# Kernel optimization log

Measured on AMD Instinct MI355X. Metric: run time of the kernel, lower is better.

The kernel has to match this reference:

```python
import jax, jax.numpy as jnp
import numpy as np

N = 20000      # nodes
E = 320000     # edges (before self loops)
DIN = 64       # input feature dim
C = 256        # hidden_dim (per-head channels)
HEADS = 4
NEG_SLOPE_ATT = 0.2   # GATv2 leaky_relu slope
NEG_SLOPE = 0.01      # torch F.leaky_relu default


def setup_inputs() -> dict:
    key = jax.random.key(0)
    ks = jax.random.split(key, 32)
    def g(i, shape, fan_in):
        return jax.random.normal(ks[i], shape, jnp.float32) * (1.0 / np.sqrt(fan_in))
    inp = {}
    inp["x"] = jax.random.normal(ks[0], (N, DIN), jnp.float32)
    inp["src"] = jax.random.randint(ks[1], (E,), 0, N, jnp.int32)
    inp["dst"] = jax.random.randint(ks[2], (E,), 0, N, jnp.int32)
    # input layer
    inp["W_in"] = g(3, (DIN, C), DIN); inp["b_in"] = jnp.zeros((C,), jnp.float32)
    # conv1: in=256 -> heads=4, out=256, concat
    inp["Wl1"] = g(4, (C, HEADS * C), C); inp["bl1"] = jnp.zeros((HEADS * C,), jnp.float32)
    inp["Wr1"] = g(5, (C, HEADS * C), C); inp["br1"] = jnp.zeros((HEADS * C,), jnp.float32)
    inp["att1"] = g(6, (HEADS, C), C); inp["bias1"] = jnp.zeros((HEADS * C,), jnp.float32)
    # conv2: in=1024 -> heads=4, out=256, concat
    inp["Wl2"] = g(7, (HEADS * C, HEADS * C), HEADS * C); inp["bl2"] = jnp.zeros((HEADS * C,), jnp.float32)
    inp["Wr2"] = g(8, (HEADS * C, HEADS * C), HEADS * C); inp["br2"] = jnp.zeros((HEADS * C,), jnp.float32)
    inp["att2"] = g(9, (HEADS, C), C); inp["bias2"] = jnp.zeros((HEADS * C,), jnp.float32)
    # conv3: in=1024 -> heads=1, out=256, no concat
    inp["Wl3"] = g(10, (HEADS * C, C), HEADS * C); inp["bl3"] = jnp.zeros((C,), jnp.float32)
    inp["Wr3"] = g(11, (HEADS * C, C), HEADS * C); inp["br3"] = jnp.zeros((C,), jnp.float32)
    inp["att3"] = g(12, (1, C), C); inp["bias3"] = jnp.zeros((C,), jnp.float32)
    # output layer
    inp["W_out"] = g(13, (C, 1), C); inp["b_out"] = jnp.zeros((1,), jnp.float32)
    return inp


def _seg_softmax(scores, seg, n):
    # scores: [E, H] segment-wise softmax over dst node ids
    m = jax.ops.segment_max(scores, seg, num_segments=n)
    ex = jnp.exp(scores - m[seg])
    den = jax.ops.segment_sum(ex, seg, num_segments=n)
    return ex / den[seg]


def _gatv2(x, s, d, Wl, bl, Wr, br, att, bias, heads, concat):
    n = x.shape[0]
    c = att.shape[1]
    xl = (x @ Wl + bl).reshape(n, heads, c)  # messages (source side)
    xr = (x @ Wr + br).reshape(n, heads, c)  # target side
    e = jax.nn.leaky_relu(xl[s] + xr[d], NEG_SLOPE_ATT)          # [E, H, C]
    sc = jnp.einsum('ehc,hc->eh', e, att)                         # [E, H]
    alpha = _seg_softmax(sc, d, n)                                # [E, H]
    out = jax.ops.segment_sum(alpha[:, :, None] * xl[s], d, num_segments=n)  # [N, H, C]
    out = out.reshape(n, heads * c) if concat else out.mean(axis=1)
    return out + bias


def reference(x, src, dst, W_in, b_in, Wl1, bl1, Wr1, br1, att1, bias1,
              Wl2, bl2, Wr2, br2, att2, bias2, Wl3, bl3, Wr3, br3, att3, bias3,
              W_out, b_out):
    n = x.shape[0]
    loop = jnp.arange(n, dtype=src.dtype)
    s = jnp.concatenate([src, loop])  # add_self_loops=True (PyG default)
    d = jnp.concatenate([dst, loop])
    h = jax.nn.leaky_relu(x @ W_in + b_in, NEG_SLOPE)
    h1 = jax.nn.elu(_gatv2(h, s, d, Wl1, bl1, Wr1, br1, att1, bias1, HEADS, True))
    h2 = jax.nn.elu(_gatv2(h1, s, d, Wl2, bl2, Wr2, br2, att2, bias2, HEADS, True))
    h3 = _gatv2(h2, s, d, Wl3, bl3, Wr3, br3, att3, bias3, 1, False)
    out = jax.nn.leaky_relu(h3, NEG_SLOPE) + h
    logits = (out @ W_out + b_out).squeeze(-1)
    return logits
```

## Files before the change

kernel.cpp:

```cpp
#include <hip/hip_runtime.h>
#include <math.h>

#define NEG_ATT 0.2f
#define NEG 0.01f

typedef __attribute__((ext_vector_type(8))) short short8;
typedef __attribute__((ext_vector_type(4))) float f32x4;

static __device__ __forceinline__ float lrelu(float x, float s) { return x > 0.f ? x : s * x; }
static __device__ __forceinline__ unsigned short f2b(float f) {
  union { float f; unsigned int i; } v; v.f = f;
  unsigned int r = (v.i + 0x7fffu + ((v.i >> 16) & 1u)) >> 16;
  return (unsigned short)r;
}
static __device__ __forceinline__ void unpack8(uint4 r, float* x) {
  union { unsigned int u; float f; } t;
  t.u = r.x << 16;          x[0] = t.f;
  t.u = r.x & 0xffff0000u;  x[1] = t.f;
  t.u = r.y << 16;          x[2] = t.f;
  t.u = r.y & 0xffff0000u;  x[3] = t.f;
  t.u = r.z << 16;          x[4] = t.f;
  t.u = r.z & 0xffff0000u;  x[5] = t.f;
  t.u = r.w << 16;          x[6] = t.f;
  t.u = r.w & 0xffff0000u;  x[7] = t.f;
}

__global__ void zero_int_kernel(int* __restrict__ p, int n) {
  int i = blockIdx.x * blockDim.x + threadIdx.x;
  if (i < n) p[i] = 0;
}

__global__ void hist_kernel(const int* __restrict__ dst, int* __restrict__ cnt, int E, int N) {
  int i = blockIdx.x * blockDim.x + threadIdx.x;
  int tot = E + N;
  if (i >= tot) return;
  int d = (i < E) ? dst[i] : (i - E);
  atomicAdd(&cnt[d], 1);
}

__global__ void scan_kernel(const int* __restrict__ cnt, int* __restrict__ rowptr,
                            int* __restrict__ cursor, int n) {
  __shared__ int wsum[16];
  __shared__ int carry_s;
  int t = threadIdx.x;
  int lane = t & 63, wv = t >> 6;
  if (t == 0) carry_s = 0;
  __syncthreads();
  for (int base = 0; base < n; base += 1024) {
    int i = base + t;
    int orig = (i < n) ? cnt[i] : 0;
    int v = orig;
    #pragma unroll
    for (int off = 1; off < 64; off <<= 1) {
      int u = __shfl_up(v, off);
      if (lane >= off) v += u;
    }
    if (lane == 63) wsum[wv] = v;
    __syncthreads();
    if (t < 16) {
      int s = wsum[t];
      #pragma unroll
      for (int off = 1; off < 16; off <<= 1) {
        int u = __shfl_up(s, off);
        if (t >= off) s += u;
      }
      wsum[t] = s;
    }
    __syncthreads();
    int waveoff = (wv > 0) ? wsum[wv - 1] : 0;
    int carry = carry_s;
    int excl = carry + waveoff + v - orig;
    if (i < n) { rowptr[i] = excl; cursor[i] = excl; }
    __syncthreads();
    if (t == 0) carry_s = carry + wsum[15];
    __syncthreads();
  }
  if (t == 0) rowptr[n] = carry_s;
}

__global__ void fill_kernel(const int* __restrict__ src, const int* __restrict__ dst,
                            int* __restrict__ cursor, int* __restrict__ colsrc, int E, int N) {
  int i = blockIdx.x * blockDim.x + threadIdx.x;
  int tot = E + N;
  if (i >= tot) return;
  int d, s;
  if (i < E) { d = dst[i]; s = src[i]; } else { d = i - E; s = i - E; }
  int pos = atomicAdd(&cursor[d], 1);
  colsrc[pos] = s;
}

__global__ __launch_bounds__(256) void transpose_w_bf16(
    const float* __restrict__ W, unsigned short* __restrict__ Wt, int K, int Ncol) {
  __shared__ float t[32][33];
  int n0 = blockIdx.x * 32, k0 = blockIdx.y * 32;
  int tx = threadIdx.x & 31, ty = threadIdx.x >> 5;
  #pragma unroll
  for (int i = 0; i < 4; ++i)
    t[ty + i * 8][tx] = W[(size_t)(k0 + ty + i * 8) * Ncol + n0 + tx];
  __syncthreads();
  #pragma unroll
  for (int i = 0; i < 4; ++i)
    Wt[(size_t)(n0 + ty + i * 8) * K + k0 + tx] = f2b(t[tx][ty + i * 8]);
}

__global__ void f2b_kernel(const float* __restrict__ in, unsigned short* __restrict__ out, int n) {
  int i = blockIdx.x * blockDim.x + threadIdx.x;
  if (i < n) out[i] = f2b(in[i]);
}

__global__ __launch_bounds__(256) void gemm_mfma(
    const unsigned short* __restrict__ A, const unsigned short* __restrict__ Bt,
    const float* __restrict__ bias, float* __restrict__ Cf, unsigned short* __restrict__ Cb,
    int M, int K, int ldcf, int ldcb, int act) {
  __shared__ __align__(16) unsigned short As[128 * 32];
  __shared__ __align__(16) unsigned short Bs[128 * 32];
  int tid = threadIdx.x;
  int wave = tid >> 6, lane = tid & 63;
  int wm = wave >> 1, wn = wave & 1;
  int quad = lane >> 4, l16 = lane & 15;
  int row0 = blockIdx.y * 128, col0 = blockIdx.x * 128;
  int r0 = tid >> 2, seg0 = tid & 3;
  int swz0 = r0 * 32 + ((seg0 ^ ((r0 >> 1) & 3)) * 8);
  int swz1 = swz0 + 64 * 32;
  int chunk = (quad ^ ((l16 >> 1) & 3)) * 8;

  const unsigned short* gA = A + (size_t)(row0 + r0) * K + seg0 * 8;
  const unsigned short* gB = Bt + (size_t)(col0 + r0) * K + seg0 * 8;
  const size_t rstep = (size_t)64 * K;

  f32x4 acc[4][4];
  #pragma unroll
  for (int i = 0; i < 4; ++i)
    #pragma unroll
    for (int j = 0; j < 4; ++j)
      acc[i][j] = (f32x4){0.f, 0.f, 0.f, 0.f};

  uint4 sa0 = *(const uint4*)(gA);
  uint4 sa1 = *(const uint4*)(gA + rstep);
  uint4 sb0 = *(const uint4*)(gB);
  uint4 sb1 = *(const uint4*)(gB + rstep);

  for (int k0 = 0; k0 < K; k0 += 32) {
    *(uint4*)&As[swz0] = sa0;
    *(uint4*)&As[swz1] = sa1;
    *(uint4*)&Bs[swz0] = sb0;
    *(uint4*)&Bs[swz1] = sb1;
    __syncthreads();
    int kn = k0 + 32;
    if (kn < K) {
      sa0 = *(const uint4*)(gA + kn);
      sa1 = *(const uint4*)(gA + kn + rstep);
      sb0 = *(const uint4*)(gB + kn);
      sb1 = *(const uint4*)(gB + kn + rstep);
    }
    short8 afr[4], bfr[4];
    #pragma unroll
    for (int t = 0; t < 4; ++t) {
      afr[t] = *(const short8*)&As[(wm * 64 + t * 16 + l16) * 32 + chunk];
      bfr[t] = *(const short8*)&Bs[(wn * 64 + t * 16 + l16) * 32 + chunk];
    }
    #pragma unroll
    for (int mt = 0; mt < 4; ++mt)
      #pragma unroll
      for (int nt = 0; nt < 4; ++nt)
        acc[mt][nt] = __builtin_amdgcn_mfma_f32_16x16x32_bf16(afr[mt], bfr[nt], acc[mt][nt], 0, 0, 0);
    __syncthreads();
  }

  #pragma unroll
  for (int mt = 0; mt < 4; ++mt) {
    #pragma unroll
    for (int r = 0; r < 4; ++r) {
      int row = row0 + wm * 64 + mt * 16 + quad * 4 + r;
      if (row >= M) continue;
      #pragma unroll
      for (int nt = 0; nt < 4; ++nt) {
        int col = col0 + wn * 64 + nt * 16 + l16;
        float v = acc[mt][nt][r] + bias[col];
        if (act == 1) v = lrelu(v, NEG);
        if (Cf) Cf[(size_t)row * ldcf + col] = v;
        if (Cb) Cb[(size_t)row * ldcb + col] = f2b(v);
      }
    }
  }
}

__global__ __launch_bounds__(256) void gat_agg_h4(
    const unsigned short* __restrict__ xlr,
    const int* __restrict__ rowptr, const int* __restrict__ colsrc,
    const float* __restrict__ att, const float* __restrict__ bias,
    unsigned short* __restrict__ outb, int n) {
  const int S = 2048, XROFF = 1024;
  int d = blockIdx.x;
  if (d >= n) return;
  int hd = threadIdx.x >> 6, ln = threadIdx.x & 63;
  int half = ln >> 5, l32 = ln & 31;
  int c0 = l32 * 8;
  float a[8], a5[8], xr_[8];
  {
    float4 t0 = *(const float4*)(att + hd * 256 + c0);
    float4 t1 = *(const float4*)(att + hd * 256 + c0 + 4);
    a[0]=t0.x; a[1]=t0.y; a[2]=t0.z; a[3]=t0.w;
    a[4]=t1.x; a[5]=t1.y; a[6]=t1.z; a[7]=t1.w;
    #pragma unroll
    for (int c = 0; c < 8; ++c) a5[c] = NEG_ATT * a[c];
    uint4 r = *(const uint4*)(xlr + (size_t)d * S + XROFF + hd * 256 + c0);
    unpack8(r, xr_);
  }
  float m = -1e30f, l = 0.f, acc[8];
  #pragma unroll
  for (int c = 0; c < 8; ++c) acc[c] = 0.f;
  int beg = rowptr[d], end = rowptr[d + 1];
  for (int j = beg; j < end; j += 2) {
    int jj = j + half;
    bool valid = (jj < end);
    int s = colsrc[valid ? jj : j];
    uint4 raw = *(const uint4*)(xlr + (size_t)s * S + hd * 256 + c0);
    float x[8];
    unpack8(raw, x);
    float p = 0.f;
    #pragma unroll
    for (int c = 0; c < 8; ++c) {
      float u = x[c] + xr_[c];
      p = fmaf(u, (u > 0.f ? a[c] : a5[c]), p);
    }
    #pragma unroll
    for (int off = 16; off >= 1; off >>= 1) p += __shfl_xor(p, off);
    if (!valid) p = -1e30f;
    float nm = fmaxf(m, p);
    if (nm > m) {
      float scl = __expf(m - nm);
      l *= scl;
      #pragma unroll
      for (int c = 0; c < 8; ++c) acc[c] *= scl;
      m = nm;
    }
    float w = __expf(p - m);
    l += w;
    #pragma unroll
    for (int c = 0; c < 8; ++c) acc[c] = fmaf(w, x[c], acc[c]);
  }
  float mo = __shfl_xor(m, 32);
  float lo = __shfl_xor(l, 32);
  float M = fmaxf(m, mo);
  float sl = __expf(m - M);
  float so = __expf(mo - M);
  float L = fmaf(l, sl, lo * so);
  float inv = 1.f / L;
  float4 b0 = *(const float4*)(bias + hd * 256 + c0);
  float4 b1 = *(const float4*)(bias + hd * 256 + c0 + 4);
  float bb[8] = {b0.x, b0.y, b0.z, b0.w, b1.x, b1.y, b1.z, b1.w};
  unsigned int ou[4];
  #pragma unroll
  for (int c = 0; c < 8; ++c) {
    float po = __shfl_xor(acc[c], 32);
    float v = fmaf(acc[c], sl, po * so) * inv + bb[c];
    v = v > 0.f ? v : expm1f(v);
    unsigned int bv = (unsigned int)f2b(v);
    if (c & 1) ou[c >> 1] |= bv << 16; else ou[c >> 1] = bv;
  }
  if (half == 0) {
    uint4 o = make_uint4(ou[0], ou[1], ou[2], ou[3]);
    *(uint4*)(outb + (size_t)d * 1024 + hd * 256 + c0) = o;
  }
}

__global__ __launch_bounds__(256) void gat_agg_h1(
    const unsigned short* __restrict__ xlr,
    const int* __restrict__ rowptr, const int* __restrict__ colsrc,
    const float* __restrict__ att, const float* __restrict__ bias,
    float* __restrict__ out, int n) {
  const int S = 512, XROFF = 256;
  int wv = threadIdx.x >> 6, ln = threadIdx.x & 63;
  int d = blockIdx.x * 4 + wv;
  if (d >= n) return;
  int half = ln >> 5, l32 = ln & 31;
  int c0 = l32 * 8;
  float a[8], a5[8], xr_[8];
  {
    float4 t0 = *(const float4*)(att + c0);
    float4 t1 = *(const float4*)(att + c0 + 4);
    a[0]=t0.x; a[1]=t0.y; a[2]=t0.z; a[3]=t0.w;
    a[4]=t1.x; a[5]=t1.y; a[6]=t1.z; a[7]=t1.w;
    #pragma unroll
    for (int c = 0; c < 8; ++c) a5[c] = NEG_ATT * a[c];
    uint4 r = *(const uint4*)(xlr + (size_t)d * S + XROFF + c0);
    unpack8(r, xr_);
  }
  float m = -1e30f, l = 0.f, acc[8];
  #pragma unroll
  for (int c = 0; c < 8; ++c) acc[c] = 0.f;
  int beg = rowptr[d], end = rowptr[d + 1];
  for (int j = beg; j < end; j += 2) {
    int jj = j + half;
    bool valid = (jj < end);
    int s = colsrc[valid ? jj : j];
    uint4 raw = *(const uint4*)(xlr + (size_t)s * S + c0);
    float x[8];
    unpack8(raw, x);
    float p = 0.f;
    #pragma unroll
    for (int c = 0; c < 8; ++c) {
      float u = x[c] + xr_[c];
      p = fmaf(u, (u > 0.f ? a[c] : a5[c]), p);
    }
    #pragma unroll
    for (int off = 16; off >= 1; off >>= 1) p += __shfl_xor(p, off);
    if (!valid) p = -1e30f;
    float nm = fmaxf(m, p);
    if (nm > m) {
      float scl = __expf(m - nm);
      l *= scl;
      #pragma unroll
      for (int c = 0; c < 8; ++c) acc[c] *= scl;
      m = nm;
    }
    float w = __expf(p - m);
    l += w;
    #pragma unroll
    for (int c = 0; c < 8; ++c) acc[c] = fmaf(w, x[c], acc[c]);
  }
  float mo = __shfl_xor(m, 32);
  float lo = __shfl_xor(l, 32);
  float M = fmaxf(m, mo);
  float sl = __expf(m - M);
  float so = __expf(mo - M);
  float L = fmaf(l, sl, lo * so);
  float inv = 1.f / L;
  float4 b0 = *(const float4*)(bias + c0);
  float4 b1 = *(const float4*)(bias + c0 + 4);
  float bb[8] = {b0.x, b0.y, b0.z, b0.w, b1.x, b1.y, b1.z, b1.w};
  float ov[8];
  #pragma unroll
  for (int c = 0; c < 8; ++c) {
    float po = __shfl_xor(acc[c], 32);
    ov[c] = fmaf(acc[c], sl, po * so) * inv + bb[c];
  }
  if (half == 0) {
    float4 o0 = {ov[0], ov[1], ov[2], ov[3]};
    float4 o1 = {ov[4], ov[5], ov[6], ov[7]};
    *(float4*)(out + (size_t)d * 256 + c0) = o0;
    *(float4*)(out + (size_t)d * 256 + c0 + 4) = o1;
  }
}

__global__ __launch_bounds__(256) void final_logits(
    const float* __restrict__ h3, const float* __restrict__ h,
    const float* __restrict__ Wout, const float* __restrict__ bout,
    float* __restrict__ out, int n) {
  int wv = threadIdx.x >> 6, ln = threadIdx.x & 63;
  int node = blockIdx.x * 4 + wv;
  if (node >= n) return;
  int c0 = ln * 4;
  float4 a = *(const float4*)(h3 + (size_t)node * 256 + c0);
  float4 b = *(const float4*)(h + (size_t)node * 256 + c0);
  float4 w = *(const float4*)(Wout + c0);
  float vx = lrelu(a.x, NEG) + b.x;
  float vy = lrelu(a.y, NEG) + b.y;
  float vz = lrelu(a.z, NEG) + b.z;
  float vw = lrelu(a.w, NEG) + b.w;
  float v = vx * w.x + vy * w.y + vz * w.z + vw * w.w;
  #pragma unroll
  for (int off = 32; off >= 1; off >>= 1) v += __shfl_xor(v, off);
  if (ln == 0) out[node] = v + bout[0];
}

extern "C" void kernel_launch(void* const* d_in, const int* in_sizes, int n_in,
                              void* d_out, int out_size, void* d_ws, size_t ws_size,
                              hipStream_t stream) {
  const float* x    = (const float*)d_in[0];
  const int*   src  = (const int*)d_in[1];
  const int*   dst  = (const int*)d_in[2];
  const float* W_in = (const float*)d_in[3];
  const float* b_in = (const float*)d_in[4];
  const float* Wl1 = (const float*)d_in[5];  const float* bl1 = (const float*)d_in[6];
  const float* Wr1 = (const float*)d_in[7];  const float* br1 = (const float*)d_in[8];
  const float* att1 = (const float*)d_in[9]; const float* bias1 = (const float*)d_in[10];
  const float* Wl2 = (const float*)d_in[11]; const float* bl2 = (const float*)d_in[12];
  const float* Wr2 = (const float*)d_in[13]; const float* br2 = (const float*)d_in[14];
  const float* att2 = (const float*)d_in[15]; const float* bias2 = (const float*)d_in[16];
  const float* Wl3 = (const float*)d_in[17]; const float* bl3 = (const float*)d_in[18];
  const float* Wr3 = (const float*)d_in[19]; const float* br3 = (const float*)d_in[20];
  const float* att3 = (const float*)d_in[21]; const float* bias3 = (const float*)d_in[22];
  const float* W_out = (const float*)d_in[23]; const float* b_out = (const float*)d_in[24];

  const int N = in_sizes[0] / 64;
  const int E = in_sizes[1];
  const int NP = ((N + 127) / 128) * 128;
  float* out = (float*)d_out;

  char* p = (char*)d_ws;
  float* h   = (float*)p;            p += (size_t)N * 256 * 4;
  float* h3  = (float*)p;            p += (size_t)N * 256 * 4;
  unsigned short* xbf  = (unsigned short*)p; p += (size_t)NP * 64 * 2;
  unsigned short* hbf  = (unsigned short*)p; p += (size_t)NP * 256 * 2;
  unsigned short* h1bf = (unsigned short*)p; p += (size_t)NP * 1024 * 2;
  unsigned short* h2bf = (unsigned short*)p; p += (size_t)NP * 1024 * 2;
  unsigned short* xlr  = (unsigned short*)p; p += (size_t)N * 2048 * 2;
  unsigned short* WtIn  = (unsigned short*)p; p += (size_t)256 * 64 * 2;
  unsigned short* WtLR1 = (unsigned short*)p; p += (size_t)2048 * 256 * 2;
  unsigned short* WtLR2 = (unsigned short*)p; p += (size_t)2048 * 1024 * 2;
  unsigned short* WtLR3 = (unsigned short*)p; p += (size_t)512 * 1024 * 2;
  float* bLR1 = (float*)p;           p += (size_t)2048 * 4;
  float* bLR2 = (float*)p;           p += (size_t)2048 * 4;
  float* bLR3 = (float*)p;           p += (size_t)512 * 4;
  int* cnt    = (int*)p;             p += (size_t)N * 4;
  int* cursor = (int*)p;             p += (size_t)N * 4;
  int* rowptr = (int*)p;             p += (size_t)(N + 1) * 4;
  int* colsrc = (int*)p;

  const int tot = E + N;
  dim3 blk(256);

  zero_int_kernel<<<(N + 255) / 256, blk, 0, stream>>>(cnt, N);
  hist_kernel<<<(tot + 255) / 256, blk, 0, stream>>>(dst, cnt, E, N);
  scan_kernel<<<1, 1024, 0, stream>>>(cnt, rowptr, cursor, N);
  fill_kernel<<<(tot + 255) / 256, blk, 0, stream>>>(src, dst, cursor, colsrc, E, N);

  transpose_w_bf16<<<dim3(8, 2), blk, 0, stream>>>(W_in, WtIn, 64, 256);
  transpose_w_bf16<<<dim3(32, 8), blk, 0, stream>>>(Wl1, WtLR1, 256, 1024);
  transpose_w_bf16<<<dim3(32, 8), blk, 0, stream>>>(Wr1, WtLR1 + (size_t)1024 * 256, 256, 1024);
  transpose_w_bf16<<<dim3(32, 32), blk, 0, stream>>>(Wl2, WtLR2, 1024, 1024);
  transpose_w_bf16<<<dim3(32, 32), blk, 0, stream>>>(Wr2, WtLR2 + (size_t)1024 * 1024, 1024, 1024);
  transpose_w_bf16<<<dim3(8, 32), blk, 0, stream>>>(Wl3, WtLR3, 1024, 256);
  transpose_w_bf16<<<dim3(8, 32), blk, 0, stream>>>(Wr3, WtLR3 + (size_t)256 * 1024, 1024, 256);
  f2b_kernel<<<(N * 64 + 255) / 256, blk, 0, stream>>>(x, xbf, N * 64);

  hipMemcpyAsync(bLR1, bl1, 1024 * 4, hipMemcpyDeviceToDevice, stream);
  hipMemcpyAsync(bLR1 + 1024, br1, 1024 * 4, hipMemcpyDeviceToDevice, stream);
  hipMemcpyAsync(bLR2, bl2, 1024 * 4, hipMemcpyDeviceToDevice, stream);
  hipMemcpyAsync(bLR2 + 1024, br2, 1024 * 4, hipMemcpyDeviceToDevice, stream);
  hipMemcpyAsync(bLR3, bl3, 256 * 4, hipMemcpyDeviceToDevice, stream);
  hipMemcpyAsync(bLR3 + 256, br3, 256 * 4, hipMemcpyDeviceToDevice, stream);

  int gy = NP / 128;
  int gagg4 = N;
  int gagg1 = (N + 3) / 4;

  gemm_mfma<<<dim3(2, gy), blk, 0, stream>>>(xbf, WtIn, b_in, h, hbf, N, 64, 256, 256, 1);

  gemm_mfma<<<dim3(16, gy), blk, 0, stream>>>(hbf, WtLR1, bLR1, nullptr, xlr, N, 256, 0, 2048, 0);
  gat_agg_h4<<<gagg4, blk, 0, stream>>>(xlr, rowptr, colsrc, att1, bias1, h1bf, N);

  gemm_mfma<<<dim3(16, gy), blk, 0, stream>>>(h1bf, WtLR2, bLR2, nullptr, xlr, N, 1024, 0, 2048, 0);
  gat_agg_h4<<<gagg4, blk, 0, stream>>>(xlr, rowptr, colsrc, att2, bias2, h2bf, N);

  gemm_mfma<<<dim3(4, gy), blk, 0, stream>>>(h2bf, WtLR3, bLR3, nullptr, xlr, N, 1024, 0, 512, 0);
  gat_agg_h1<<<gagg1, blk, 0, stream>>>(xlr, rowptr, colsrc, att3, bias3, h3, N);

  final_logits<<<gagg1, blk, 0, stream>>>(h3, h, W_out, b_out, out, N);
}
```

Measured before the change: 784.2 us.

## Fuse prep kernels, widen GEMM K-tile to 64, fuse final logits into aggregation

Weight transposes, bias copies and x conversion are merged into one launch, replacing eight kernels and six memcpys. The MFMA GEMM now stages a 64-wide K slice per iteration, halving barrier and loop overhead at the cost of doubled LDS and more prefetch registers. The last GAT aggregation directly computes the residual, leaky-relu and output dot product, removing the h3 intermediate buffer and a separate kernel.

```diff
diff --git a/kernel.cpp b/kernel.cpp
--- a/kernel.cpp
+++ b/kernel.cpp
@@ -89,10 +89,12 @@
   colsrc[pos] = s;
 }
 
-__global__ __launch_bounds__(256) void transpose_w_bf16(
-    const float* __restrict__ W, unsigned short* __restrict__ Wt, int K, int Ncol) {
-  __shared__ float t[32][33];
-  int n0 = blockIdx.x * 32, k0 = blockIdx.y * 32;
+static __device__ __forceinline__ void do_transpose(
+    const float* __restrict__ W, unsigned short* __restrict__ Wt,
+    int K, int Ncol, int lbid, float (*t)[33]) {
+  int nxb = Ncol >> 5;
+  int bx = lbid % nxb, by = lbid / nxb;
+  int n0 = bx * 32, k0 = by * 32;
   int tx = threadIdx.x & 31, ty = threadIdx.x >> 5;
   #pragma unroll
   for (int i = 0; i < 4; ++i)
@@ -103,26 +105,61 @@
     Wt[(size_t)(n0 + ty + i * 8) * K + k0 + tx] = f2b(t[tx][ty + i * 8]);
 }
 
-__global__ void f2b_kernel(const float* __restrict__ in, unsigned short* __restrict__ out, int n) {
-  int i = blockIdx.x * blockDim.x + threadIdx.x;
-  if (i < n) out[i] = f2b(in[i]);
+__global__ __launch_bounds__(256) void prep_all(
+    const float* __restrict__ W_in,
+    const float* __restrict__ Wl1, const float* __restrict__ Wr1,
+    const float* __restrict__ Wl2, const float* __restrict__ Wr2,
+    const float* __restrict__ Wl3, const float* __restrict__ Wr3,
+    unsigned short* __restrict__ WtIn,
+    unsigned short* __restrict__ WtL1, unsigned short* __restrict__ WtR1,
+    unsigned short* __restrict__ WtL2, unsigned short* __restrict__ WtR2,
+    unsigned short* __restrict__ WtL3, unsigned short* __restrict__ WtR3,
+    const float* __restrict__ x, unsigned short* __restrict__ xbf, int nx_elems,
+    const float* __restrict__ bl1, const float* __restrict__ br1,
+    const float* __restrict__ bl2, const float* __restrict__ br2,
+    const float* __restrict__ bl3, const float* __restrict__ br3,
+    float* __restrict__ bLR1, float* __restrict__ bLR2, float* __restrict__ bLR3) {
+  __shared__ float t[32][33];
+  int bid = blockIdx.x;
+  if (bid < 16)        { do_transpose(W_in, WtIn, 64, 256, bid, t); return; }
+  if (bid < 272)       { do_transpose(Wl1, WtL1, 256, 1024, bid - 16, t); return; }
+  if (bid < 528)       { do_transpose(Wr1, WtR1, 256, 1024, bid - 272, t); return; }
+  if (bid < 1552)      { do_transpose(Wl2, WtL2, 1024, 1024, bid - 528, t); return; }
+  if (bid < 2576)      { do_transpose(Wr2, WtR2, 1024, 1024, bid - 1552, t); return; }
+  if (bid < 2832)      { do_transpose(Wl3, WtL3, 1024, 256, bid - 2576, t); return; }
+  if (bid < 3088)      { do_transpose(Wr3, WtR3, 1024, 256, bid - 2832, t); return; }
+  if (bid < 3106) {
+    int i = (bid - 3088) * 256 + threadIdx.x;
+    if (i < 1024)      bLR1[i] = bl1[i];
+    else if (i < 2048) bLR1[i] = br1[i - 1024];
+    else if (i < 3072) bLR2[i - 2048] = bl2[i - 2048];
+    else if (i < 4096) bLR2[i - 2048] = br2[i - 3072];
+    else if (i < 4352) bLR3[i - 4096] = bl3[i - 4096];
+    else if (i < 4608) bLR3[i - 4096] = br3[i - 4352];
+    return;
+  }
+  int i = (bid - 3106) * 256 + threadIdx.x;
+  if (i < nx_elems) xbf[i] = f2b(x[i]);
 }
 
 __global__ __launch_bounds__(256) void gemm_mfma(
     const unsigned short* __restrict__ A, const unsigned short* __restrict__ Bt,
     const float* __restrict__ bias, float* __restrict__ Cf, unsigned short* __restrict__ Cb,
     int M, int K, int ldcf, int ldcb, int act) {
-  __shared__ __align__(16) unsigned short As[128 * 32];
-  __shared__ __align__(16) unsigned short Bs[128 * 32];
+  __shared__ __align__(16) unsigned short As[128 * 64];
+  __shared__ __align__(16) unsigned short Bs[128 * 64];
   int tid = threadIdx.x;
   int wave = tid >> 6, lane = tid & 63;
   int wm = wave >> 1, wn = wave & 1;
   int quad = lane >> 4, l16 = lane & 15;
   int row0 = blockIdx.y * 128, col0 = blockIdx.x * 128;
   int r0 = tid >> 2, seg0 = tid & 3;
-  int swz0 = r0 * 32 + ((seg0 ^ ((r0 >> 1) & 3)) * 8);
-  int swz1 = swz0 + 64 * 32;
-  int chunk = (quad ^ ((l16 >> 1) & 3)) * 8;
+  int swz = (seg0 ^ ((r0 >> 1) & 3)) * 8;
+  int wsl0 = r0 * 64 + swz;
+  int wsl1 = wsl0 + 32;
+  int wsl2 = wsl0 + 64 * 64;
+  int wsl3 = wsl2 + 32;
+  int chunkbase = (quad ^ ((l16 >> 1) & 3)) * 8;
 
   const unsigned short* gA = A + (size_t)(row0 + r0) * K + seg0 * 8;
   const unsigned short* gB = Bt + (size_t)(col0 + r0) * K + seg0 * 8;
@@ -135,35 +172,50 @@
     for (int j = 0; j < 4; ++j)
       acc[i][j] = (f32x4){0.f, 0.f, 0.f, 0.f};
 
-  uint4 sa0 = *(const uint4*)(gA);
-  uint4 sa1 = *(const uint4*)(gA + rstep);
-  uint4 sb0 = *(const uint4*)(gB);
-  uint4 sb1 = *(const uint4*)(gB + rstep);
-
-  for (int k0 = 0; k0 < K; k0 += 32) {
-    *(uint4*)&As[swz0] = sa0;
-    *(uint4*)&As[swz1] = sa1;
-    *(uint4*)&Bs[swz0] = sb0;
-    *(uint4*)&Bs[swz1] = sb1;
-    __syncthreads();
-    int kn = k0 + 32;
+  uint4 pa0 = *(const uint4*)(gA);
+  uint4 pa1 = *(const uint4*)(gA + 32);
+  uint4 pa2 = *(const uint4*)(gA + rstep);
+  uint4 pa3 = *(const uint4*)(gA + rstep + 32);
+  uint4 pb0 = *(const uint4*)(gB);
+  uint4 pb1 = *(const uint4*)(gB + 32);
+  uint4 pb2 = *(const uint4*)(gB + rstep);
+  uint4 pb3 = *(const uint4*)(gB + rstep + 32);
+
+  for (int k0 = 0; k0 < K; k0 += 64) {
+    *(uint4*)&As[wsl0] = pa0;
+    *(uint4*)&As[wsl1] = pa1;
+    *(uint4*)&As[wsl2] = pa2;
+    *(uint4*)&As[wsl3] = pa3;
+    *(uint4*)&Bs[wsl0] = pb0;
+    *(uint4*)&Bs[wsl1] = pb1;
+    *(uint4*)&Bs[wsl2] = pb2;
+    *(uint4*)&Bs[wsl3] = pb3;
+    __syncthreads();
+    int kn = k0 + 64;
     if (kn < K) {
-      sa0 = *(const uint4*)(gA + kn);
-      sa1 = *(const uint4*)(gA + kn + rstep);
-      sb0 = *(const uint4*)(gB + kn);
-      sb1 = *(const uint4*)(gB + kn + rstep);
-    }
-    short8 afr[4], bfr[4];
-    #pragma unroll
-    for (int t = 0; t < 4; ++t) {
-      afr[t] = *(const short8*)&As[(wm * 64 + t * 16 + l16) * 32 + chunk];
-      bfr[t] = *(const short8*)&Bs[(wn * 64 + t * 16 + l16) * 32 + chunk];
-    }
-    #pragma unroll
-    for (int mt = 0; mt < 4; ++mt)
-      #pragma unroll
-      for (int nt = 0; nt < 4; ++nt)
-        acc[mt][nt] = __builtin_amdgcn_mfma_f32_16x16x32_bf16(afr[mt], bfr[nt], acc[mt][nt], 0, 0, 0);
+      pa0 = *(const uint4*)(gA + kn);
+      pa1 = *(const uint4*)(gA + kn + 32);
+      pa2 = *(const uint4*)(gA + kn + rstep);
+      pa3 = *(const uint4*)(gA + kn + rstep + 32);
+      pb0 = *(const uint4*)(gB + kn);
+      pb1 = *(const uint4*)(gB + kn + 32);
+      pb2 = *(const uint4*)(gB + kn + rstep);
+      pb3 = *(const uint4*)(gB + kn + rstep + 32);
+    }
+    #pragma unroll
+    for (int h = 0; h < 2; ++h) {
+      short8 afr[4], bfr[4];
+      #pragma unroll
+      for (int t = 0; t < 4; ++t) {
+        afr[t] = *(const short8*)&As[(wm * 64 + t * 16 + l16) * 64 + h * 32 + chunkbase];
+        bfr[t] = *(const short8*)&Bs[(wn * 64 + t * 16 + l16) * 64 + h * 32 + chunkbase];
+      }
+      #pragma unroll
+      for (int mt = 0; mt < 4; ++mt)
+        #pragma unroll
+        for (int nt = 0; nt < 4; ++nt)
+          acc[mt][nt] = __builtin_amdgcn_mfma_f32_16x16x32_bf16(afr[mt], bfr[nt], acc[mt][nt], 0, 0, 0);
+    }
     __syncthreads();
   }
 
@@ -265,11 +317,12 @@
   }
 }
 
-__global__ __launch_bounds__(256) void gat_agg_h1(
+__global__ __launch_bounds__(256) void gat_agg_h1_final(
     const unsigned short* __restrict__ xlr,
     const int* __restrict__ rowptr, const int* __restrict__ colsrc,
     const float* __restrict__ att, const float* __restrict__ bias,
-    float* __restrict__ out, int n) {
+    const float* __restrict__ h, const float* __restrict__ Wout,
+    const float* __restrict__ bout, float* __restrict__ out, int n) {
   const int S = 512, XROFF = 256;
   int wv = threadIdx.x >> 6, ln = threadIdx.x & 63;
   int d = blockIdx.x * 4 + wv;
@@ -330,39 +383,21 @@
   float4 b0 = *(const float4*)(bias + c0);
   float4 b1 = *(const float4*)(bias + c0 + 4);
   float bb[8] = {b0.x, b0.y, b0.z, b0.w, b1.x, b1.y, b1.z, b1.w};
-  float ov[8];
+  float4 h0 = *(const float4*)(h + (size_t)d * 256 + c0);
+  float4 h1v = *(const float4*)(h + (size_t)d * 256 + c0 + 4);
+  float hh[8] = {h0.x, h0.y, h0.z, h0.w, h1v.x, h1v.y, h1v.z, h1v.w};
+  float4 w0 = *(const float4*)(Wout + c0);
+  float4 w1 = *(const float4*)(Wout + c0 + 4);
+  float ww[8] = {w0.x, w0.y, w0.z, w0.w, w1.x, w1.y, w1.z, w1.w};
+  float v = 0.f;
   #pragma unroll
   for (int c = 0; c < 8; ++c) {
-    float po = __shfl_xor(acc[c], 32);
-    ov[c] = fmaf(acc[c], sl, po * so) * inv + bb[c];
-  }
-  if (half == 0) {
-    float4 o0 = {ov[0], ov[1], ov[2], ov[3]};
-    float4 o1 = {ov[4], ov[5], ov[6], ov[7]};
-    *(float4*)(out + (size_t)d * 256 + c0) = o0;
-    *(float4*)(out + (size_t)d * 256 + c0 + 4) = o1;
-  }
-}
-
-__global__ __launch_bounds__(256) void final_logits(
-    const float* __restrict__ h3, const float* __restrict__ h,
-    const float* __restrict__ Wout, const float* __restrict__ bout,
-    float* __restrict__ out, int n) {
-  int wv = threadIdx.x >> 6, ln = threadIdx.x & 63;
-  int node = blockIdx.x * 4 + wv;
-  if (node >= n) return;
-  int c0 = ln * 4;
-  float4 a = *(const float4*)(h3 + (size_t)node * 256 + c0);
-  float4 b = *(const float4*)(h + (size_t)node * 256 + c0);
-  float4 w = *(const float4*)(Wout + c0);
-  float vx = lrelu(a.x, NEG) + b.x;
-  float vy = lrelu(a.y, NEG) + b.y;
-  float vz = lrelu(a.z, NEG) + b.z;
-  float vw = lrelu(a.w, NEG) + b.w;
-  float v = vx * w.x + vy * w.y + vz * w.z + vw * w.w;
-  #pragma unroll
-  for (int off = 32; off >= 1; off >>= 1) v += __shfl_xor(v, off);
-  if (ln == 0) out[node] = v + bout[0];
+    float h3c = fmaf(acc[c], sl, __shfl_xor(acc[c], 32) * so) * inv + bb[c];
+    v = fmaf(lrelu(h3c, NEG) + hh[c], ww[c], v);
+  }
+  #pragma unroll
+  for (int off = 16; off >= 1; off >>= 1) v += __shfl_xor(v, off);
+  if (ln == 0) out[d] = v + bout[0];
 }
 
 extern "C" void kernel_launch(void* const* d_in, const int* in_sizes, int n_in,
@@ -391,7 +426,6 @@
 
   char* p = (char*)d_ws;
   float* h   = (float*)p;            p += (size_t)N * 256 * 4;
-  float* h3  = (float*)p;            p += (size_t)N * 256 * 4;
   unsigned short* xbf  = (unsigned short*)p; p += (size_t)NP * 64 * 2;
   unsigned short* hbf  = (unsigned short*)p; p += (size_t)NP * 256 * 2;
   unsigned short* h1bf = (unsigned short*)p; p += (size_t)NP * 1024 * 2;
@@ -417,21 +451,14 @@
   scan_kernel<<<1, 1024, 0, stream>>>(cnt, rowptr, cursor, N);
   fill_kernel<<<(tot + 255) / 256, blk, 0, stream>>>(src, dst, cursor, colsrc, E, N);
 
-  transpose_w_bf16<<<dim3(8, 2), blk, 0, stream>>>(W_in, WtIn, 64, 256);
-  transpose_w_bf16<<<dim3(32, 8), blk, 0, stream>>>(Wl1, WtLR1, 256, 1024);
-  transpose_w_bf16<<<dim3(32, 8), blk, 0, stream>>>(Wr1, WtLR1 + (size_t)1024 * 256, 256, 1024);
-  transpose_w_bf16<<<dim3(32, 32), blk, 0, stream>>>(Wl2, WtLR2, 1024, 1024);
-  transpose_w_bf16<<<dim3(32, 32), blk, 0, stream>>>(Wr2, WtLR2 + (size_t)1024 * 1024, 1024, 1024);
-  transpose_w_bf16<<<dim3(8, 32), blk, 0, stream>>>(Wl3, WtLR3, 1024, 256);
-  transpose_w_bf16<<<dim3(8, 32), blk, 0, stream>>>(Wr3, WtLR3 + (size_t)256 * 1024, 1024, 256);
-  f2b_kernel<<<(N * 64 + 255) / 256, blk, 0, stream>>>(x, xbf, N * 64);
-
-  hipMemcpyAsync(bLR1, bl1, 1024 * 4, hipMemcpyDeviceToDevice, stream);
-  hipMemcpyAsync(bLR1 + 1024, br1, 1024 * 4, hipMemcpyDeviceToDevice, stream);
-  hipMemcpyAsync(bLR2, bl2, 1024 * 4, hipMemcpyDeviceToDevice, stream);
-  hipMemcpyAsync(bLR2 + 1024, br2, 1024 * 4, hipMemcpyDeviceToDevice, stream);
-  hipMemcpyAsync(bLR3, bl3, 256 * 4, hipMemcpyDeviceToDevice, stream);
-  hipMemcpyAsync(bLR3 + 256, br3, 256 * 4, hipMemcpyDeviceToDevice, stream);
+  int nbf2b = (N * 64 + 255) / 256;
+  prep_all<<<3106 + nbf2b, blk, 0, stream>>>(
+      W_in, Wl1, Wr1, Wl2, Wr2, Wl3, Wr3,
+      WtIn, WtLR1, WtLR1 + (size_t)1024 * 256,
+      WtLR2, WtLR2 + (size_t)1024 * 1024,
+      WtLR3, WtLR3 + (size_t)256 * 1024,
+      x, xbf, N * 64,
+      bl1, br1, bl2, br2, bl3, br3, bLR1, bLR2, bLR3);
 
   int gy = NP / 128;
   int gagg4 = N;
@@ -446,7 +473,6 @@
   gat_agg_h4<<<gagg4, blk, 0, stream>>>(xlr, rowptr, colsrc, att2, bias2, h2bf, N);
 
   gemm_mfma<<<dim3(4, gy), blk, 0, stream>>>(h2bf, WtLR3, bLR3, nullptr, xlr, N, 1024, 0, 512, 0);
-  gat_agg_h1<<<gagg1, blk, 0, stream>>>(xlr, rowptr, colsrc, att3, bias3, h3, N);
-
-  final_logits<<<gagg1, blk, 0, stream>>>(h3, h, W_out, b_out, out, N);
-}
+  gat_agg_h1_final<<<gagg1, blk, 0, stream>>>(xlr, rowptr, colsrc, att3, bias3,
+                                              h, W_out, b_out, out, N);
+}
```

Result: faster. 741.9 us (-5.4%).
